# Kernel tuning notes

Measured on AMD Instinct MI355X. Metric: run time of the kernel, lower is better.

## Reference

```python
import jax, jax.numpy as jnp
import numpy as np

EMBED_DIM = 1024
N_HEADS = 16
HEAD_DIM = EMBED_DIM // N_HEADS


def setup_inputs() -> dict:
    key = jax.random.key(0)
    k1, k2, k3 = jax.random.split(key, 3)
    B, T, C = 2, 2048, EMBED_DIM
    x = jax.random.normal(k1, (B, T, C), dtype=jnp.float32)
    # nn.Linear-style init scale
    s = 1.0 / np.sqrt(C)
    Wqkv = jax.random.normal(k2, (C, 3 * C), dtype=jnp.float32) * s
    bqkv = jnp.zeros((3 * C,), dtype=jnp.float32)
    Wout = jax.random.normal(k3, (C, C), dtype=jnp.float32) * s
    bout = jnp.zeros((C,), dtype=jnp.float32)
    return {"x": x, "Wqkv": Wqkv, "bqkv": bqkv, "Wout": Wout, "bout": bout}


def reference(x, Wqkv, bqkv, Wout, bout):
    B, T, C = x.shape
    H, D = N_HEADS, HEAD_DIM
    qkv = x @ Wqkv + bqkv  # [B,T,3C]
    q, k, v = jnp.split(qkv, 3, axis=-1)
    # [B,T,C] -> [B,H,T,D]
    q = q.reshape(B, T, H, D).transpose(0, 2, 1, 3)
    k = k.reshape(B, T, H, D).transpose(0, 2, 1, 3)
    v = v.reshape(B, T, H, D).transpose(0, 2, 1, 3)
    scale = 1.0 / np.sqrt(D)
    scores = jnp.einsum("bhqd,bhkd->bhqk", q, k) * scale  # [B,H,T,T]
    causal = jnp.tril(jnp.ones((T, T), dtype=bool))  # True where allowed
    scores = jnp.where(causal, scores, jnp.finfo(scores.dtype).min)
    attn = jax.nn.softmax(scores, axis=-1)
    out = jnp.einsum("bhqk,bhkd->bhqd", attn, v)  # [B,H,T,D]
    out = out.transpose(0, 2, 1, 3).reshape(B, T, C)
    return out @ Wout + bout
```

## Files before the change

kernel.cpp:

```cpp
#include <hip/hip_runtime.h>
#include <hip/hip_bf16.h>
#include <stdint.h>

#define EMBED 1024
#define NH 16
#define HD 64
#define BATCH 2
#define SEQ 2048
#define MTOK (BATCH*SEQ)

using bf8 = __attribute__((ext_vector_type(8))) short;
using f4  = __attribute__((ext_vector_type(4))) float;
using f16v = __attribute__((ext_vector_type(16))) float;
using u16x4 = __attribute__((ext_vector_type(4))) unsigned short;

union U4 { uint32_t u[4]; bf8 v; };

#define S_BIAS 12.0f

__device__ __forceinline__ uint32_t pk_bf16(float a, float b) {
  __hip_bfloat162 h = __float22bfloat162_rn(float2{a, b});
  union { __hip_bfloat162 h; uint32_t u; } c; c.h = h; return c.u;
}
__device__ __forceinline__ unsigned short bfbits(float f) {
  __hip_bfloat16 h = __float2bfloat16(f);
  union { __hip_bfloat16 h; unsigned short u; } c; c.h = h; return c.u;
}
__device__ __forceinline__ float bf2f(unsigned short u) {
  union { uint32_t u; float f; } c; c.u = (uint32_t)u << 16; return c.f;
}
__device__ __forceinline__ float fexp2(float x) {
#if __has_builtin(__builtin_amdgcn_exp2f)
  return __builtin_amdgcn_exp2f(x);
#else
  return exp2f(x);
#endif
}
__device__ __forceinline__ float frcp(float x) {
#if __has_builtin(__builtin_amdgcn_rcpf)
  return __builtin_amdgcn_rcpf(x);
#else
  return 1.f / x;
#endif
}

__device__ __forceinline__ void gl2lds16(const void* g, void* l) {
  __builtin_amdgcn_global_load_lds(
      (const __attribute__((address_space(1))) void*)g,
      (__attribute__((address_space(3))) void*)l, 16, 0, 0);
}

__global__ __launch_bounds__(256) void conv_bf16(const float* __restrict__ x,
                                                 unsigned short* __restrict__ y) {
  int i = (blockIdx.x * 256 + threadIdx.x) * 4;
  float4 v = *(const float4*)(x + i);
  uint2 o;
  o.x = pk_bf16(v.x, v.y);
  o.y = pk_bf16(v.z, v.w);
  *(uint2*)(y + i) = o;
}

__global__ __launch_bounds__(256) void transp_bf16(const float* __restrict__ W,
                                                   unsigned short* __restrict__ Wt,
                                                   int K, int N) {
  __shared__ float tl[64][65];
  int k0 = blockIdx.y * 64, n0 = blockIdx.x * 64;
  int tr = threadIdx.x >> 6, tc = threadIdx.x & 63;
#pragma unroll
  for (int i = 0; i < 16; i++) {
    int r = tr + i * 4;
    tl[r][tc] = W[(size_t)(k0 + r) * N + n0 + tc];
  }
  __syncthreads();
#pragma unroll
  for (int i = 0; i < 16; i++) {
    int r = tr + i * 4;
    Wt[(size_t)(n0 + r) * K + k0 + tc] = bfbits(tl[tc][r]);
  }
}

template<int BN, int MODE>
__global__ __launch_bounds__(256) void gemm_bt(const unsigned short* __restrict__ A,
                                               const unsigned short* __restrict__ Bt,
                                               const float* __restrict__ bias,
                                               unsigned short* __restrict__ Oq,
                                               unsigned short* __restrict__ Ov,
                                               float* __restrict__ Of,
                                               int M, int N, int K) {
  constexpr int MT = (BN == 128) ? 4 : 2;
  const int tid = threadIdx.x;
  const int w = tid >> 6, lane = tid & 63;
  const int wm = (BN == 128) ? (w >> 1) : w;
  const int wn = (BN == 128) ? (w & 1) : 0;

  const int NB_N = N / BN;
  const int NB_M = M / 128;
  const int flat = blockIdx.x;
  const int xcd = flat & 7, loc = flat >> 3;
  const int m_idx = xcd * (NB_M / 8) + loc / NB_N;
  const int n_idx = loc % NB_N;
  const int m0 = m_idx * 128, n0 = n_idx * BN;

  __shared__ char smem[16384 + BN * 128];
  char* Al = smem;
  char* Bl = smem + 16384;

  f4 acc[MT][4] = {};

  for (int k0 = 0; k0 < K; k0 += 64) {
    __syncthreads();
#pragma unroll
    for (int i = 0; i < 4; i++) {
      int row = w * 8 + i * 32 + (lane >> 3);
      int col = ((lane & 7) * 8) ^ ((row & 7) << 3);
      gl2lds16(A + (size_t)(m0 + row) * K + k0 + col, Al + (w * 8 + i * 32) * 128);
    }
#pragma unroll
    for (int i = 0; i < BN / 32; i++) {
      int row = w * 8 + i * 32 + (lane >> 3);
      int col = ((lane & 7) * 8) ^ ((row & 7) << 3);
      gl2lds16(Bt + (size_t)(n0 + row) * K + k0 + col, Bl + (w * 8 + i * 32) * 128);
    }
    __syncthreads();
#pragma unroll
    for (int ks = 0; ks < 2; ks++) {
      bf8 af[MT], bfr[4];
#pragma unroll
      for (int mt = 0; mt < MT; mt++) {
        int rr = wm * (MT * 16) + mt * 16 + (lane & 15);
        af[mt] = *(const bf8*)(Al + rr * 128 + ((ks * 64 + (lane >> 4) * 16) ^ ((rr & 7) << 4)));
      }
#pragma unroll
      for (int nt = 0; nt < 4; nt++) {
        int rr = wn * 64 + nt * 16 + (lane & 15);
        bfr[nt] = *(const bf8*)(Bl + rr * 128 + ((ks * 64 + (lane >> 4) * 16) ^ ((rr & 7) << 4)));
      }
#pragma unroll
      for (int mt = 0; mt < MT; mt++)
#pragma unroll
        for (int nt = 0; nt < 4; nt++)
          acc[mt][nt] = __builtin_amdgcn_mfma_f32_16x16x32_bf16(af[mt], bfr[nt], acc[mt][nt], 0, 0, 0);
    }
  }

  if (MODE == 0) {
    const int region = n0 >> 10;
    if (region < 2) {
      float sc = (region == 0) ? 0.180336880f : 1.0f;
#pragma unroll
      for (int nt = 0; nt < 4; nt++) {
        int n = n0 + wn * 64 + nt * 16 + (lane & 15);
        float bv = bias[n];
        int c = n & 1023, h = c >> 6, d = c & 63;
#pragma unroll
        for (int mt = 0; mt < MT; mt++) {
#pragma unroll
          for (int r = 0; r < 4; r++) {
            int m = m0 + wm * (MT * 16) + mt * 16 + (lane >> 4) * 4 + r;
            int b = m >> 11, t = m & 2047;
            size_t off = ((((size_t)region * 2 + b) * 16 + h) * 2048 + t) * 64 + d;
            Oq[off] = bfbits((acc[mt][nt][r] + bv) * sc);
          }
        }
      }
    } else {
#pragma unroll
      for (int nt = 0; nt < 4; nt++) {
        int n = n0 + wn * 64 + nt * 16 + (lane & 15);
        float bv = bias[n];
        int c = n & 1023, h = c >> 6, d = c & 63;
#pragma unroll
        for (int mt = 0; mt < MT; mt++) {
          int m = m0 + wm * (MT * 16) + mt * 16 + (lane >> 4) * 4;
          int b = m >> 11, t = m & 2047;
          size_t off = (((size_t)b * 16 + h) * 64 + d) * 2048 + t;
          u16x4 pk4;
#pragma unroll
          for (int r = 0; r < 4; r++) pk4[r] = bfbits(acc[mt][nt][r] + bv);
          *(u16x4*)(Ov + off) = pk4;
        }
      }
    }
  } else {
#pragma unroll
    for (int mt = 0; mt < MT; mt++) {
#pragma unroll
      for (int r = 0; r < 4; r++) {
        int m = m0 + wm * (MT * 16) + mt * 16 + (lane >> 4) * 4 + r;
#pragma unroll
        for (int nt = 0; nt < 4; nt++) {
          int n = n0 + wn * 64 + nt * 16 + (lane & 15);
          Of[(size_t)m * N + n] = acc[mt][nt][r] + bias[n];
        }
      }
    }
  }
}

__global__ __launch_bounds__(256) void attn8(const unsigned short* __restrict__ Qb,
                                             const unsigned short* __restrict__ Kb,
                                             const unsigned short* __restrict__ Vtb,
                                             unsigned short* __restrict__ Ob,
                                             unsigned short* __restrict__ partO,
                                             float2* __restrict__ ML) {
  const int idx = blockIdx.x;
  int qt, ts, te;
  const int bh = idx & 31;
  if (idx < 256)        { qt = 8 + (idx >> 5);          ts = 0;  te = 16; }
  else if (idx < 512)   { qt = 8 + ((idx - 256) >> 5);  ts = 16; te = 2 * qt + 2; }
  else                  { qt = 7 - ((idx - 512) >> 5);  ts = 0;  te = 2 * qt + 2; }

  const int tid = threadIdx.x;
  const int w = tid >> 6, lane = tid & 63;
  const int hi = lane >> 5, q32 = lane & 31;

  __shared__ char smem[32768];

  const unsigned short* Qg  = Qb  + (size_t)bh * SEQ * HD;
  const unsigned short* Kg  = Kb  + (size_t)bh * SEQ * HD;
  const unsigned short* Vtg = Vtb + (size_t)bh * SEQ * HD;

  const int qbw  = qt * 128 + w * 32;
  const int qrow = qbw + q32;

  bf8 qf[4];
#pragma unroll
  for (int kc = 0; kc < 4; kc++)
    qf[kc] = *(const bf8*)(Qg + (size_t)qrow * HD + kc * 16 + hi * 8);

  U4 ones;
#pragma unroll
  for (int i = 0; i < 4; i++) ones.u[i] = 0x3F803F80u;

  f16v acc0 = {}, acc1 = {}, accl = {};

  auto STAGE = [&](int buf, int t) {
    int kv0 = t * 64;
#pragma unroll
    for (int i = 0; i < 2; i++) {
      int c = i * 4 + w;
      int row = c * 8 + (lane >> 3);
      int col = ((lane & 7) * 8) ^ ((row & 7) << 3);
      gl2lds16(Kg + (size_t)(kv0 + row) * HD + col,    smem + buf * 8192 + c * 1024);
      gl2lds16(Vtg + (size_t)row * SEQ + kv0 + col,    smem + 16384 + buf * 8192 + c * 1024);
    }
  };

  STAGE(0, ts);
  __syncthreads();

  const int nt_loc = te - ts;
  for (int tl = 0; tl < nt_loc; tl++) {
    const int t = ts + tl;
    if (tl + 1 < nt_loc) STAGE((tl + 1) & 1, t + 1);
    const int kv0 = t * 64;

    if (kv0 <= qbw + 31) {
      const char* kl = smem + (tl & 1) * 8192;
      const char* vl = smem + 16384 + (tl & 1) * 8192;
      const bool hi_vis = (kv0 + 32 <= qbw + 31);

      f16v s0, s1;
#pragma unroll
      for (int r = 0; r < 16; r++) { s0[r] = -S_BIAS; s1[r] = -S_BIAS; }
      __builtin_amdgcn_s_setprio(1);
#pragma unroll
      for (int kc = 0; kc < 4; kc++) {
        int r0 = q32;
        bf8 k0 = *(const bf8*)(kl + r0 * 128 + ((kc * 32 + hi * 16) ^ ((r0 & 7) << 4)));
        s0 = __builtin_amdgcn_mfma_f32_32x32x16_bf16(k0, qf[kc], s0, 0, 0, 0);
      }
      if (hi_vis) {
#pragma unroll
        for (int kc = 0; kc < 4; kc++) {
          int r1 = 32 + q32;
          bf8 k1 = *(const bf8*)(kl + r1 * 128 + ((kc * 32 + hi * 16) ^ ((r1 & 7) << 4)));
          s1 = __builtin_amdgcn_mfma_f32_32x32x16_bf16(k1, qf[kc], s1, 0, 0, 0);
        }
      }
      __builtin_amdgcn_s_setprio(0);

      if (kv0 + 63 > qbw) {
#pragma unroll
        for (int r = 0; r < 16; r++) {
          int key = kv0 + (r & 3) + 8 * (r >> 2) + 4 * hi;
          if (key > qrow)      s0[r] = -1e30f;
          if (key + 32 > qrow) s1[r] = -1e30f;
        }
      }

      uint32_t u[16];
#pragma unroll
      for (int m8 = 0; m8 < 8; m8++) {
        float pa = fexp2(s0[2 * m8]), pb = fexp2(s0[2 * m8 + 1]);
        u[m8] = pk_bf16(pa, pb);
      }
      if (hi_vis) {
#pragma unroll
        for (int m8 = 0; m8 < 8; m8++) {
          float pc = fexp2(s1[2 * m8]), pd = fexp2(s1[2 * m8 + 1]);
          u[8 + m8] = pk_bf16(pc, pd);
        }
      }

      __builtin_amdgcn_s_setprio(1);
      const int ncc = hi_vis ? 4 : 2;
      for (int kcc = 0; kcc < ncc; kcc++) {
        const int base = (kcc >> 1) * 8 + (kcc & 1) * 4;
        uint32_t a0 = u[base + 0], a2 = u[base + 2];
        uint32_t a1 = u[base + 1], a3 = u[base + 3];
        asm("v_permlane32_swap_b32 %0, %1" : "+v"(a0), "+v"(a2));
        asm("v_permlane32_swap_b32 %0, %1" : "+v"(a1), "+v"(a3));
        U4 f; f.u[0] = a0; f.u[1] = a1; f.u[2] = a2; f.u[3] = a3;
        int r0 = q32, r1 = 32 + q32;
        bf8 v0 = *(const bf8*)(vl + r0 * 128 + ((kcc * 32 + hi * 16) ^ ((r0 & 7) << 4)));
        bf8 v1 = *(const bf8*)(vl + r1 * 128 + ((kcc * 32 + hi * 16) ^ ((r1 & 7) << 4)));
        acc0 = __builtin_amdgcn_mfma_f32_32x32x16_bf16(f.v, v0, acc0, 0, 0, 0);
        acc1 = __builtin_amdgcn_mfma_f32_32x32x16_bf16(f.v, v1, acc1, 0, 0, 0);
        accl = __builtin_amdgcn_mfma_f32_32x32x16_bf16(f.v, ones.v, accl, 0, 0, 0);
      }
      __builtin_amdgcn_s_setprio(0);
    }
    __syncthreads();
  }

  if (qt < 8) {
    int b = bh >> 4, h = bh & 15;
    unsigned short* Og = Ob + (size_t)b * SEQ * EMBED;
#pragma unroll
    for (int r = 0; r < 16; r++) {
      int ql_ = (r & 3) + 8 * (r >> 2) + 4 * hi;
      float linv = frcp(accl[r]);
      size_t rowoff = (size_t)(qbw + ql_) * EMBED + h * 64;
      Og[rowoff + q32]      = bfbits(acc0[r] * linv);
      Og[rowoff + 32 + q32] = bfbits(acc1[r] * linv);
    }
  } else {
    int seg = (ts == 16) ? 1 : 0;
    int part = ((qt - 8) * 32 + bh) * 2 + seg;
    unsigned short* P0 = partO + (size_t)part * 8192;
#pragma unroll
    for (int r = 0; r < 16; r++) {
      int ql_ = (r & 3) + 8 * (r >> 2) + 4 * hi;
      int rowl = w * 32 + ql_;
      P0[rowl * 64 + q32]      = bfbits(acc0[r]);
      P0[rowl * 64 + 32 + q32] = bfbits(acc1[r]);
    }
    if (q32 == 0) {
#pragma unroll
      for (int r = 0; r < 16; r++) {
        int ql_ = (r & 3) + 8 * (r >> 2) + 4 * hi;
        ML[part * 128 + w * 32 + ql_] = float2{S_BIAS, accl[r]};
      }
    }
  }
}

__global__ __launch_bounds__(256) void attn_combine(const unsigned short* __restrict__ partO,
                                                    const float2* __restrict__ ML,
                                                    unsigned short* __restrict__ Ob) {
  int pair = blockIdx.x;
  int qt = 8 + (pair >> 5), bh = pair & 31;
  int p0 = pair * 2, p1 = p0 + 1;
  int b = bh >> 4, h = bh & 15;
#pragma unroll
  for (int rr = 0; rr < 2; rr++) {
    int row = rr * 64 + (threadIdx.x >> 2);
    int d0 = (threadIdx.x & 3) * 16;
    float2 ml0 = ML[p0 * 128 + row], ml1 = ML[p1 * 128 + row];
    float m = fmaxf(ml0.x, ml1.x);
    float w0 = fexp2(ml0.x - m), w1 = fexp2(ml1.x - m);
    float linv = 1.f / (w0 * ml0.y + w1 * ml1.y);
    w0 *= linv; w1 *= linv;
    const unsigned short* O0 = partO + (size_t)p0 * 8192 + row * 64 + d0;
    const unsigned short* O1 = partO + (size_t)p1 * 8192 + row * 64 + d0;
    unsigned short* out = Ob + ((size_t)b * SEQ + qt * 128 + row) * EMBED + h * 64 + d0;
    u16x4 res[4];
#pragma unroll
    for (int v = 0; v < 4; v++) {
      u16x4 a = *(const u16x4*)(O0 + v * 4);
      u16x4 c = *(const u16x4*)(O1 + v * 4);
#pragma unroll
      for (int e = 0; e < 4; e++)
        res[v][e] = bfbits(w0 * bf2f(a[e]) + w1 * bf2f(c[e]));
    }
    *(u16x4*)(out)      = res[0];
    *(u16x4*)(out + 4)  = res[1];
    *(u16x4*)(out + 8)  = res[2];
    *(u16x4*)(out + 12) = res[3];
  }
}

extern "C" void kernel_launch(void* const* d_in, const int* in_sizes, int n_in,
                              void* d_out, int out_size, void* d_ws, size_t ws_size,
                              hipStream_t stream) {
  const float* x    = (const float*)d_in[0];
  const float* Wqkv = (const float*)d_in[1];
  const float* bqkv = (const float*)d_in[2];
  const float* Wout = (const float*)d_in[3];
  const float* bout = (const float*)d_in[4];
  float* out = (float*)d_out;

  char* ws = (char*)d_ws;
  unsigned short* xb    = (unsigned short*)ws;
  unsigned short* partO = (unsigned short*)ws;
  unsigned short* wqkvT = (unsigned short*)(ws + (size_t)8  * 1048576);
  float2*         mlbuf = (float2*)(ws + (size_t)8 * 1048576);
  unsigned short* woutT = (unsigned short*)(ws + (size_t)14 * 1048576);
  unsigned short* qk    = (unsigned short*)(ws + (size_t)16 * 1048576);
  unsigned short* vT    = (unsigned short*)(ws + (size_t)32 * 1048576);
  unsigned short* obuf  = (unsigned short*)(ws + (size_t)40 * 1048576);

  conv_bf16<<<4096, 256, 0, stream>>>(x, xb);
  transp_bf16<<<dim3(48, 16), 256, 0, stream>>>(Wqkv, wqkvT, 1024, 3072);
  transp_bf16<<<dim3(16, 16), 256, 0, stream>>>(Wout, woutT, 1024, 1024);

  gemm_bt<128, 0><<<dim3(768), 256, 0, stream>>>(xb, wqkvT, bqkv, qk, vT, nullptr,
                                                 MTOK, 3 * EMBED, EMBED);

  const unsigned short* Qb = qk;
  const unsigned short* Kb = qk + (size_t)BATCH * NH * SEQ * HD;
  attn8<<<dim3(768), 256, 0, stream>>>(Qb, Kb, vT, obuf, partO, mlbuf);
  attn_combine<<<dim3(256), 256, 0, stream>>>(partO, mlbuf, obuf);

  gemm_bt<64, 1><<<dim3(512), 256, 0, stream>>>(obuf, woutT, bout, nullptr, nullptr, out,
                                                MTOK, EMBED, EMBED);
}
```

Measured before the change: 120.9 us.

## Fuse prep kernels into one launch and drop XCD-aware GEMM tile mapping

Merges the activation conversion and the two weight transposes into a single prep kernel that dispatches on block index, cutting two kernel launches. The GEMM grid goes from a flat XCD-swizzled mapping to a plain 2D grid, which gives up the L2 locality the swizzle provided. The QKV epilogue is unified into one loop that writes V as scalar strided stores instead of packed 4-element vectors, so V stores become less coalesced.

```diff
diff --git a/kernel.cpp b/kernel.cpp
--- a/kernel.cpp
+++ b/kernel.cpp
@@ -50,21 +50,32 @@
       (__attribute__((address_space(3))) void*)l, 16, 0, 0);
 }
 
-__global__ __launch_bounds__(256) void conv_bf16(const float* __restrict__ x,
-                                                 unsigned short* __restrict__ y) {
-  int i = (blockIdx.x * 256 + threadIdx.x) * 4;
-  float4 v = *(const float4*)(x + i);
-  uint2 o;
-  o.x = pk_bf16(v.x, v.y);
-  o.y = pk_bf16(v.z, v.w);
-  *(uint2*)(y + i) = o;
-}
-
-__global__ __launch_bounds__(256) void transp_bf16(const float* __restrict__ W,
-                                                   unsigned short* __restrict__ Wt,
-                                                   int K, int N) {
+__global__ __launch_bounds__(256) void prep(const float* __restrict__ x,
+                                            unsigned short* __restrict__ xb,
+                                            const float* __restrict__ Wqkv,
+                                            unsigned short* __restrict__ wqkvT,
+                                            const float* __restrict__ Wout,
+                                            unsigned short* __restrict__ woutT) {
   __shared__ float tl[64][65];
-  int k0 = blockIdx.y * 64, n0 = blockIdx.x * 64;
+  int blk = blockIdx.x;
+  if (blk < 4096) {
+    int i = (blk * 256 + threadIdx.x) * 4;
+    float4 v = *(const float4*)(x + i);
+    uint2 o;
+    o.x = pk_bf16(v.x, v.y);
+    o.y = pk_bf16(v.z, v.w);
+    *(uint2*)(xb + i) = o;
+    return;
+  }
+  const float* W; unsigned short* Wt; int K, N, bx, by;
+  if (blk < 4096 + 768) {
+    int j = blk - 4096; W = Wqkv; Wt = wqkvT; K = 1024; N = 3072;
+    bx = j % 48; by = j / 48;
+  } else {
+    int j = blk - 4096 - 768; W = Wout; Wt = woutT; K = 1024; N = 1024;
+    bx = j % 16; by = j / 16;
+  }
+  int k0 = by * 64, n0 = bx * 64;
   int tr = threadIdx.x >> 6, tc = threadIdx.x & 63;
 #pragma unroll
   for (int i = 0; i < 16; i++) {
@@ -92,14 +103,7 @@
   const int w = tid >> 6, lane = tid & 63;
   const int wm = (BN == 128) ? (w >> 1) : w;
   const int wn = (BN == 128) ? (w & 1) : 0;
-
-  const int NB_N = N / BN;
-  const int NB_M = M / 128;
-  const int flat = blockIdx.x;
-  const int xcd = flat & 7, loc = flat >> 3;
-  const int m_idx = xcd * (NB_M / 8) + loc / NB_N;
-  const int n_idx = loc % NB_N;
-  const int m0 = m_idx * 128, n0 = n_idx * BN;
+  const int m0 = blockIdx.y * 128, n0 = blockIdx.x * BN;
 
   __shared__ char smem[16384 + BN * 128];
   char* Al = smem;
@@ -144,40 +148,26 @@
   }
 
   if (MODE == 0) {
-    const int region = n0 >> 10;
-    if (region < 2) {
+#pragma unroll
+    for (int nt = 0; nt < 4; nt++) {
+      int n = n0 + wn * 64 + nt * 16 + (lane & 15);
+      float bv = bias[n];
+      int region = n >> 10, c = n & 1023, h = c >> 6, d = c & 63;
       float sc = (region == 0) ? 0.180336880f : 1.0f;
 #pragma unroll
-      for (int nt = 0; nt < 4; nt++) {
-        int n = n0 + wn * 64 + nt * 16 + (lane & 15);
-        float bv = bias[n];
-        int c = n & 1023, h = c >> 6, d = c & 63;
-#pragma unroll
-        for (int mt = 0; mt < MT; mt++) {
-#pragma unroll
-          for (int r = 0; r < 4; r++) {
-            int m = m0 + wm * (MT * 16) + mt * 16 + (lane >> 4) * 4 + r;
-            int b = m >> 11, t = m & 2047;
+      for (int mt = 0; mt < MT; mt++) {
+#pragma unroll
+        for (int r = 0; r < 4; r++) {
+          int m = m0 + wm * (MT * 16) + mt * 16 + (lane >> 4) * 4 + r;
+          int b = m >> 11, t = m & 2047;
+          unsigned short val = bfbits((acc[mt][nt][r] + bv) * sc);
+          if (region < 2) {
             size_t off = ((((size_t)region * 2 + b) * 16 + h) * 2048 + t) * 64 + d;
-            Oq[off] = bfbits((acc[mt][nt][r] + bv) * sc);
+            Oq[off] = val;
+          } else {
+            size_t off = (((size_t)b * 16 + h) * 64 + d) * 2048 + t;
+            Ov[off] = val;
           }
-        }
-      }
-    } else {
-#pragma unroll
-      for (int nt = 0; nt < 4; nt++) {
-        int n = n0 + wn * 64 + nt * 16 + (lane & 15);
-        float bv = bias[n];
-        int c = n & 1023, h = c >> 6, d = c & 63;
-#pragma unroll
-        for (int mt = 0; mt < MT; mt++) {
-          int m = m0 + wm * (MT * 16) + mt * 16 + (lane >> 4) * 4;
-          int b = m >> 11, t = m & 2047;
-          size_t off = (((size_t)b * 16 + h) * 64 + d) * 2048 + t;
-          u16x4 pk4;
-#pragma unroll
-          for (int r = 0; r < 4; r++) pk4[r] = bfbits(acc[mt][nt][r] + bv);
-          *(u16x4*)(Ov + off) = pk4;
         }
       }
     }
@@ -411,18 +401,16 @@
   unsigned short* vT    = (unsigned short*)(ws + (size_t)32 * 1048576);
   unsigned short* obuf  = (unsigned short*)(ws + (size_t)40 * 1048576);
 
-  conv_bf16<<<4096, 256, 0, stream>>>(x, xb);
-  transp_bf16<<<dim3(48, 16), 256, 0, stream>>>(Wqkv, wqkvT, 1024, 3072);
-  transp_bf16<<<dim3(16, 16), 256, 0, stream>>>(Wout, woutT, 1024, 1024);
-
-  gemm_bt<128, 0><<<dim3(768), 256, 0, stream>>>(xb, wqkvT, bqkv, qk, vT, nullptr,
-                                                 MTOK, 3 * EMBED, EMBED);
+  prep<<<dim3(4096 + 768 + 256), 256, 0, stream>>>(x, xb, Wqkv, wqkvT, Wout, woutT);
+
+  gemm_bt<128, 0><<<dim3(24, 32), 256, 0, stream>>>(xb, wqkvT, bqkv, qk, vT, nullptr,
+                                                    MTOK, 3 * EMBED, EMBED);
 
   const unsigned short* Qb = qk;
   const unsigned short* Kb = qk + (size_t)BATCH * NH * SEQ * HD;
   attn8<<<dim3(768), 256, 0, stream>>>(Qb, Kb, vT, obuf, partO, mlbuf);
   attn_combine<<<dim3(256), 256, 0, stream>>>(partO, mlbuf, obuf);
 
-  gemm_bt<64, 1><<<dim3(512), 256, 0, stream>>>(obuf, woutT, bout, nullptr, nullptr, out,
-                                                MTOK, EMBED, EMBED);
-}
+  gemm_bt<64, 1><<<dim3(16, 32), 256, 0, stream>>>(obuf, woutT, bout, nullptr, nullptr, out,
+                                                   MTOK, EMBED, EMBED);
+}
```

After: 115.7 us. -4.3%, faster.
